# Optimization experiments

Hardware: AMD Instinct MI355X
Metric: run time of the kernel (lower is better)

The kernel has to match this reference:

```python
import jax, jax.numpy as jnp
import numpy as np

B, H, I = 64, 4096, 14336   # batch, hidden, expert intermediate
NLUT = 4096                 # 2**L_bits, L=12
W_SCALE = 0.02              # payload['W_scale'] (same for all three here)


def _rademacher(key, shape):
    return jnp.where(jax.random.bernoulli(key, 0.5, shape), 1.0, -1.0).astype(jnp.float32)


def setup_inputs() -> dict:
    key = jax.random.key(0)
    ks = jax.random.split(key, 14)
    inp = {
        "x": jax.random.normal(ks[0], (B, H), jnp.float32),
        "lut_gate": jax.random.normal(ks[1], (NLUT,), jnp.float32) * 0.05,
        "lut_up": jax.random.normal(ks[2], (NLUT,), jnp.float32) * 0.05,
        "lut_down": jax.random.normal(ks[3], (NLUT,), jnp.float32) * 0.05,
        "gate_walks": jax.random.randint(ks[4], (I, H), 0, NLUT, jnp.int32),
        "up_walks": jax.random.randint(ks[5], (I, H), 0, NLUT, jnp.int32),
        "down_walks": jax.random.randint(ks[6], (H, I), 0, NLUT, jnp.int32),
        "gate_sign_l": _rademacher(ks[7], (I,)),
        "gate_sign_r": _rademacher(ks[8], (H,)),
        "up_sign_l": _rademacher(ks[9], (I,)),
        "up_sign_r": _rademacher(ks[10], (H,)),
        "down_sign_l": _rademacher(ks[11], (H,)),
        "down_sign_r": _rademacher(ks[12], (I,)),
    }
    return inp


def _dequant(lut, walks, sign_l, sign_r):
    # trellis-walk LUT gather per weight element, then row/col signs and scalar scale
    # walks: (out, in) int codes; lut: (NLUT,)
    return (lut[walks] * sign_l[:, None] * sign_r[None, :]) * W_SCALE


def reference(x, lut_gate, lut_up, lut_down,
              gate_walks, up_walks, down_walks,
              gate_sign_l, gate_sign_r, up_sign_l, up_sign_r,
              down_sign_l, down_sign_r):
    W_gate = _dequant(lut_gate, gate_walks, gate_sign_l, gate_sign_r)  # (I, H)
    W_up = _dequant(lut_up, up_walks, up_sign_l, up_sign_r)            # (I, H)
    W_down = _dequant(lut_down, down_walks, down_sign_l, down_sign_r)  # (H, I)
    gate_out = jax.nn.silu(x @ W_gate.T)   # (B, I)
    up_out = x @ W_up.T                    # (B, I)
    hidden = gate_out * up_out
    return hidden @ W_down.T               # (B, H)
```

## Files before the change

### kernel.cpp

```cpp
#include <hip/hip_runtime.h>
#include <hip/hip_bf16.h>

#define HD   4096
#define ID   14336
#define NB   64
#define NLUTN 4096
#define KSPLIT 4

typedef __attribute__((ext_vector_type(8))) short short8;
typedef __attribute__((ext_vector_type(4))) float f32x4;

__device__ __forceinline__ unsigned short f2bf(float f) {
  __hip_bfloat16 h = __float2bfloat16(f);
  return __builtin_bit_cast(unsigned short, h);
}

__global__ __launch_bounds__(256) void prep_kernel(
    const float* __restrict__ x, const float* __restrict__ gsr,
    const float* __restrict__ usr,
    unsigned short* __restrict__ xg, unsigned short* __restrict__ xu)
{
  int t = blockIdx.x * 256 + threadIdx.x;
  float4 xv = ((const float4*)x)[t];
  int hs = t & (HD/4 - 1);
  float4 g = ((const float4*)gsr)[hs];
  float4 u = ((const float4*)usr)[hs];
  ushort4 og = make_ushort4(f2bf(xv.x*g.x), f2bf(xv.y*g.y), f2bf(xv.z*g.z), f2bf(xv.w*g.w));
  ushort4 ou = make_ushort4(f2bf(xv.x*u.x), f2bf(xv.y*u.y), f2bf(xv.z*u.z), f2bf(xv.w*u.w));
  ((ushort4*)xg)[t] = og;
  ((ushort4*)xu)[t] = ou;
}

__global__ __launch_bounds__(64) void gate_up_kernel(
    const int* __restrict__ gw, const int* __restrict__ uw,
    const float* __restrict__ lutg_f, const float* __restrict__ lutu_f,
    const unsigned short* __restrict__ xg, const unsigned short* __restrict__ xu,
    const float* __restrict__ gsl, const float* __restrict__ usl,
    const float* __restrict__ dsr,
    unsigned short* __restrict__ hidden)
{
  __shared__ unsigned short lutg[NLUTN];
  __shared__ unsigned short lutu[NLUTN];
  const int tid = threadIdx.x;

  #pragma unroll
  for (int i = tid; i < NLUTN/4; i += 64) {
    float4 g = ((const float4*)lutg_f)[i];
    float4 u = ((const float4*)lutu_f)[i];
    ((ushort4*)lutg)[i] = make_ushort4(f2bf(g.x), f2bf(g.y), f2bf(g.z), f2bf(g.w));
    ((ushort4*)lutu)[i] = make_ushort4(f2bf(u.x), f2bf(u.y), f2bf(u.z), f2bf(u.w));
  }
  __syncthreads();

  const int col  = tid & 15;
  const int quad = tid >> 4;
  const int m0   = blockIdx.x * 16;

  const int* gp = gw + (size_t)(m0 + col) * HD + quad * 8;
  const int* up = uw + (size_t)(m0 + col) * HD + quad * 8;
  const unsigned short* xgp[4];
  const unsigned short* xup[4];
  #pragma unroll
  for (int t = 0; t < 4; ++t) {
    xgp[t] = xg + (size_t)(t*16 + col) * HD + quad * 8;
    xup[t] = xu + (size_t)(t*16 + col) * HD + quad * 8;
  }

  const f32x4 z = {0.f, 0.f, 0.f, 0.f};
  f32x4 accg[4] = {z, z, z, z};
  f32x4 accu[4] = {z, z, z, z};

  for (int k0 = 0; k0 < HD; k0 += 32) {
    int4 ga = *(const int4*)(gp + k0);
    int4 gb = *(const int4*)(gp + k0 + 4);
    int4 ua = *(const int4*)(up + k0);
    int4 ub = *(const int4*)(up + k0 + 4);

    short8 afg, afu;
    afg[0] = (short)lutg[ga.x]; afg[1] = (short)lutg[ga.y];
    afg[2] = (short)lutg[ga.z]; afg[3] = (short)lutg[ga.w];
    afg[4] = (short)lutg[gb.x]; afg[5] = (short)lutg[gb.y];
    afg[6] = (short)lutg[gb.z]; afg[7] = (short)lutg[gb.w];
    afu[0] = (short)lutu[ua.x]; afu[1] = (short)lutu[ua.y];
    afu[2] = (short)lutu[ua.z]; afu[3] = (short)lutu[ua.w];
    afu[4] = (short)lutu[ub.x]; afu[5] = (short)lutu[ub.y];
    afu[6] = (short)lutu[ub.z]; afu[7] = (short)lutu[ub.w];

    #pragma unroll
    for (int t = 0; t < 4; ++t) {
      short8 bg = __builtin_bit_cast(short8, *(const int4*)(xgp[t] + k0));
      short8 bu = __builtin_bit_cast(short8, *(const int4*)(xup[t] + k0));
      accg[t] = __builtin_amdgcn_mfma_f32_16x16x32_bf16(afg, bg, accg[t], 0, 0, 0);
      accu[t] = __builtin_amdgcn_mfma_f32_16x16x32_bf16(afu, bu, accu[t], 0, 0, 0);
    }
  }

  const int mrow = m0 + quad * 4;
  float sg[4], su[4], sd[4];
  #pragma unroll
  for (int r = 0; r < 4; ++r) {
    sg[r] = 0.02f * gsl[mrow + r];
    su[r] = 0.02f * usl[mrow + r];
    sd[r] = dsr[mrow + r];
  }
  #pragma unroll
  for (int t = 0; t < 4; ++t) {
    int b = t*16 + col;
    ushort4 hv;
    float g0 = accg[t][0] * sg[0], u0 = accu[t][0] * su[0];
    float g1 = accg[t][1] * sg[1], u1 = accu[t][1] * su[1];
    float g2 = accg[t][2] * sg[2], u2 = accu[t][2] * su[2];
    float g3 = accg[t][3] * sg[3], u3 = accu[t][3] * su[3];
    hv.x = f2bf((g0 / (1.f + __expf(-g0))) * u0 * sd[0]);
    hv.y = f2bf((g1 / (1.f + __expf(-g1))) * u1 * sd[1]);
    hv.z = f2bf((g2 / (1.f + __expf(-g2))) * u2 * sd[2]);
    hv.w = f2bf((g3 / (1.f + __expf(-g3))) * u3 * sd[3]);
    *((ushort4*)(hidden + (size_t)b * ID + mrow)) = hv;
  }
}

__global__ __launch_bounds__(64) void down_kernel(
    const int* __restrict__ dw, const float* __restrict__ lutd_f,
    const unsigned short* __restrict__ hidden,
    const float* __restrict__ dsl,
    float* __restrict__ out)
{
  __shared__ unsigned short lutd[NLUTN];
  const int tid = threadIdx.x;
  #pragma unroll
  for (int i = tid; i < NLUTN/4; i += 64) {
    float4 d = ((const float4*)lutd_f)[i];
    ((ushort4*)lutd)[i] = make_ushort4(f2bf(d.x), f2bf(d.y), f2bf(d.z), f2bf(d.w));
  }
  __syncthreads();

  const int col  = tid & 15;
  const int quad = tid >> 4;
  const int m0   = blockIdx.x * 16;
  const int kbeg = blockIdx.y * (ID / KSPLIT);
  const int kend = kbeg + (ID / KSPLIT);

  const int* dp = dw + (size_t)(m0 + col) * ID + quad * 8;
  const unsigned short* hp[4];
  #pragma unroll
  for (int t = 0; t < 4; ++t)
    hp[t] = hidden + (size_t)(t*16 + col) * ID + quad * 8;

  const f32x4 z = {0.f, 0.f, 0.f, 0.f};
  f32x4 acc[4] = {z, z, z, z};

  for (int k0 = kbeg; k0 < kend; k0 += 32) {
    int4 da = *(const int4*)(dp + k0);
    int4 db = *(const int4*)(dp + k0 + 4);
    short8 af;
    af[0] = (short)lutd[da.x]; af[1] = (short)lutd[da.y];
    af[2] = (short)lutd[da.z]; af[3] = (short)lutd[da.w];
    af[4] = (short)lutd[db.x]; af[5] = (short)lutd[db.y];
    af[6] = (short)lutd[db.z]; af[7] = (short)lutd[db.w];
    #pragma unroll
    for (int t = 0; t < 4; ++t) {
      short8 bh = __builtin_bit_cast(short8, *(const int4*)(hp[t] + k0));
      acc[t] = __builtin_amdgcn_mfma_f32_16x16x32_bf16(af, bh, acc[t], 0, 0, 0);
    }
  }

  const int mrow = m0 + quad * 4;
  float sc[4];
  #pragma unroll
  for (int r = 0; r < 4; ++r) sc[r] = 0.02f * dsl[mrow + r];
  #pragma unroll
  for (int t = 0; t < 4; ++t) {
    int b = t*16 + col;
    #pragma unroll
    for (int r = 0; r < 4; ++r)
      atomicAdd(&out[(size_t)b * HD + mrow + r], acc[t][r] * sc[r]);
  }
}

extern "C" void kernel_launch(void* const* d_in, const int* in_sizes, int n_in,
                              void* d_out, int out_size, void* d_ws, size_t ws_size,
                              hipStream_t stream) {
  const float* x    = (const float*)d_in[0];
  const float* lutg = (const float*)d_in[1];
  const float* lutu = (const float*)d_in[2];
  const float* lutd = (const float*)d_in[3];
  const int*   gw   = (const int*)d_in[4];
  const int*   uw   = (const int*)d_in[5];
  const int*   dw   = (const int*)d_in[6];
  const float* gsl  = (const float*)d_in[7];
  const float* gsr  = (const float*)d_in[8];
  const float* usl  = (const float*)d_in[9];
  const float* usr  = (const float*)d_in[10];
  const float* dsl  = (const float*)d_in[11];
  const float* dsr  = (const float*)d_in[12];
  float* out = (float*)d_out;

  unsigned short* xg     = (unsigned short*)d_ws;
  unsigned short* xu     = xg + (size_t)NB * HD;
  unsigned short* hidden = xu + (size_t)NB * HD;

  hipMemsetAsync(d_out, 0, (size_t)NB * HD * sizeof(float), stream);
  prep_kernel<<<(NB*HD/4 + 255)/256, 256, 0, stream>>>(x, gsr, usr, xg, xu);
  gate_up_kernel<<<ID/16, 64, 0, stream>>>(gw, uw, lutg, lutu, xg, xu,
                                           gsl, usl, dsr, hidden);
  down_kernel<<<dim3(HD/16, KSPLIT), 64, 0, stream>>>(dw, lutd, hidden, dsl, out);
}
```

Measured before the change: 742.0 us.

## Split K across four waves per block with LDS reduction and prefetch walk codes

Both GEMM kernels now launch 256-thread blocks where each of four waves handles a quarter of the K range, and partial accumulators are summed through shared memory before the epilogue. This amortizes the per-block LUT conversion into LDS over four times more work and raises the number of waves per CU to hide the latency of the gathers and global loads. The loops also software-prefetch the next iteration's walk-code int4 loads. The cost is extra LDS for the reduction buffers, a block-wide barrier, and an idle epilogue for three of the four waves.

```diff
diff --git a/kernel.cpp b/kernel.cpp
--- a/kernel.cpp
+++ b/kernel.cpp
@@ -31,7 +31,7 @@
   ((ushort4*)xu)[t] = ou;
 }
 
-__global__ __launch_bounds__(64) void gate_up_kernel(
+__global__ __launch_bounds__(256, 4) void gate_up_kernel(
     const int* __restrict__ gw, const int* __restrict__ uw,
     const float* __restrict__ lutg_f, const float* __restrict__ lutu_f,
     const unsigned short* __restrict__ xg, const unsigned short* __restrict__ xu,
@@ -41,10 +41,14 @@
 {
   __shared__ unsigned short lutg[NLUTN];
   __shared__ unsigned short lutu[NLUTN];
-  const int tid = threadIdx.x;
-
-  #pragma unroll
-  for (int i = tid; i < NLUTN/4; i += 64) {
+  __shared__ f32x4 red[3][8][64];
+
+  const int tid  = threadIdx.x;
+  const int lane = tid & 63;
+  const int w    = tid >> 6;
+
+  #pragma unroll
+  for (int i = tid; i < NLUTN/4; i += 256) {
     float4 g = ((const float4*)lutg_f)[i];
     float4 u = ((const float4*)lutu_f)[i];
     ((ushort4*)lutg)[i] = make_ushort4(f2bf(g.x), f2bf(g.y), f2bf(g.z), f2bf(g.w));
@@ -52,9 +56,12 @@
   }
   __syncthreads();
 
-  const int col  = tid & 15;
-  const int quad = tid >> 4;
+  const int col  = lane & 15;
+  const int quad = lane >> 4;
   const int m0   = blockIdx.x * 16;
+
+  const int kbeg = w * (HD / 4);
+  const int kend = kbeg + (HD / 4);
 
   const int* gp = gw + (size_t)(m0 + col) * HD + quad * 8;
   const int* up = uw + (size_t)(m0 + col) * HD + quad * 8;
@@ -70,21 +77,28 @@
   f32x4 accg[4] = {z, z, z, z};
   f32x4 accu[4] = {z, z, z, z};
 
-  for (int k0 = 0; k0 < HD; k0 += 32) {
-    int4 ga = *(const int4*)(gp + k0);
-    int4 gb = *(const int4*)(gp + k0 + 4);
-    int4 ua = *(const int4*)(up + k0);
-    int4 ub = *(const int4*)(up + k0 + 4);
+  int4 cga = *(const int4*)(gp + kbeg);
+  int4 cgb = *(const int4*)(gp + kbeg + 4);
+  int4 cua = *(const int4*)(up + kbeg);
+  int4 cub = *(const int4*)(up + kbeg + 4);
+
+  for (int k0 = kbeg; k0 < kend; k0 += 32) {
+    int kn = k0 + 32;
+    if (kn >= kend) kn = kbeg;
+    int4 nga = *(const int4*)(gp + kn);
+    int4 ngb = *(const int4*)(gp + kn + 4);
+    int4 nua = *(const int4*)(up + kn);
+    int4 nub = *(const int4*)(up + kn + 4);
 
     short8 afg, afu;
-    afg[0] = (short)lutg[ga.x]; afg[1] = (short)lutg[ga.y];
-    afg[2] = (short)lutg[ga.z]; afg[3] = (short)lutg[ga.w];
-    afg[4] = (short)lutg[gb.x]; afg[5] = (short)lutg[gb.y];
-    afg[6] = (short)lutg[gb.z]; afg[7] = (short)lutg[gb.w];
-    afu[0] = (short)lutu[ua.x]; afu[1] = (short)lutu[ua.y];
-    afu[2] = (short)lutu[ua.z]; afu[3] = (short)lutu[ua.w];
-    afu[4] = (short)lutu[ub.x]; afu[5] = (short)lutu[ub.y];
-    afu[6] = (short)lutu[ub.z]; afu[7] = (short)lutu[ub.w];
+    afg[0] = (short)lutg[cga.x]; afg[1] = (short)lutg[cga.y];
+    afg[2] = (short)lutg[cga.z]; afg[3] = (short)lutg[cga.w];
+    afg[4] = (short)lutg[cgb.x]; afg[5] = (short)lutg[cgb.y];
+    afg[6] = (short)lutg[cgb.z]; afg[7] = (short)lutg[cgb.w];
+    afu[0] = (short)lutu[cua.x]; afu[1] = (short)lutu[cua.y];
+    afu[2] = (short)lutu[cua.z]; afu[3] = (short)lutu[cua.w];
+    afu[4] = (short)lutu[cub.x]; afu[5] = (short)lutu[cub.y];
+    afu[6] = (short)lutu[cub.z]; afu[7] = (short)lutu[cub.w];
 
     #pragma unroll
     for (int t = 0; t < 4; ++t) {
@@ -93,52 +107,79 @@
       accg[t] = __builtin_amdgcn_mfma_f32_16x16x32_bf16(afg, bg, accg[t], 0, 0, 0);
       accu[t] = __builtin_amdgcn_mfma_f32_16x16x32_bf16(afu, bu, accu[t], 0, 0, 0);
     }
-  }
-
-  const int mrow = m0 + quad * 4;
-  float sg[4], su[4], sd[4];
-  #pragma unroll
-  for (int r = 0; r < 4; ++r) {
-    sg[r] = 0.02f * gsl[mrow + r];
-    su[r] = 0.02f * usl[mrow + r];
-    sd[r] = dsr[mrow + r];
-  }
-  #pragma unroll
-  for (int t = 0; t < 4; ++t) {
-    int b = t*16 + col;
-    ushort4 hv;
-    float g0 = accg[t][0] * sg[0], u0 = accu[t][0] * su[0];
-    float g1 = accg[t][1] * sg[1], u1 = accu[t][1] * su[1];
-    float g2 = accg[t][2] * sg[2], u2 = accu[t][2] * su[2];
-    float g3 = accg[t][3] * sg[3], u3 = accu[t][3] * su[3];
-    hv.x = f2bf((g0 / (1.f + __expf(-g0))) * u0 * sd[0]);
-    hv.y = f2bf((g1 / (1.f + __expf(-g1))) * u1 * sd[1]);
-    hv.z = f2bf((g2 / (1.f + __expf(-g2))) * u2 * sd[2]);
-    hv.w = f2bf((g3 / (1.f + __expf(-g3))) * u3 * sd[3]);
-    *((ushort4*)(hidden + (size_t)b * ID + mrow)) = hv;
-  }
-}
-
-__global__ __launch_bounds__(64) void down_kernel(
+
+    cga = nga; cgb = ngb; cua = nua; cub = nub;
+  }
+
+  if (w > 0) {
+    #pragma unroll
+    for (int t = 0; t < 4; ++t) {
+      red[w-1][t][lane]     = accg[t];
+      red[w-1][4 + t][lane] = accu[t];
+    }
+  }
+  __syncthreads();
+  if (w == 0) {
+    #pragma unroll
+    for (int ww = 0; ww < 3; ++ww) {
+      #pragma unroll
+      for (int t = 0; t < 4; ++t) {
+        accg[t] += red[ww][t][lane];
+        accu[t] += red[ww][4 + t][lane];
+      }
+    }
+
+    const int mrow = m0 + quad * 4;
+    float sg[4], su[4], sd[4];
+    #pragma unroll
+    for (int r = 0; r < 4; ++r) {
+      sg[r] = 0.02f * gsl[mrow + r];
+      su[r] = 0.02f * usl[mrow + r];
+      sd[r] = dsr[mrow + r];
+    }
+    #pragma unroll
+    for (int t = 0; t < 4; ++t) {
+      int b = t*16 + col;
+      ushort4 hv;
+      float g0 = accg[t][0] * sg[0], u0 = accu[t][0] * su[0];
+      float g1 = accg[t][1] * sg[1], u1 = accu[t][1] * su[1];
+      float g2 = accg[t][2] * sg[2], u2 = accu[t][2] * su[2];
+      float g3 = accg[t][3] * sg[3], u3 = accu[t][3] * su[3];
+      hv.x = f2bf((g0 / (1.f + __expf(-g0))) * u0 * sd[0]);
+      hv.y = f2bf((g1 / (1.f + __expf(-g1))) * u1 * sd[1]);
+      hv.z = f2bf((g2 / (1.f + __expf(-g2))) * u2 * sd[2]);
+      hv.w = f2bf((g3 / (1.f + __expf(-g3))) * u3 * sd[3]);
+      *((ushort4*)(hidden + (size_t)b * ID + mrow)) = hv;
+    }
+  }
+}
+
+__global__ __launch_bounds__(256, 4) void down_kernel(
     const int* __restrict__ dw, const float* __restrict__ lutd_f,
     const unsigned short* __restrict__ hidden,
     const float* __restrict__ dsl,
     float* __restrict__ out)
 {
   __shared__ unsigned short lutd[NLUTN];
-  const int tid = threadIdx.x;
-  #pragma unroll
-  for (int i = tid; i < NLUTN/4; i += 64) {
+  __shared__ f32x4 red[3][4][64];
+
+  const int tid  = threadIdx.x;
+  const int lane = tid & 63;
+  const int w    = tid >> 6;
+
+  #pragma unroll
+  for (int i = tid; i < NLUTN/4; i += 256) {
     float4 d = ((const float4*)lutd_f)[i];
     ((ushort4*)lutd)[i] = make_ushort4(f2bf(d.x), f2bf(d.y), f2bf(d.z), f2bf(d.w));
   }
   __syncthreads();
 
-  const int col  = tid & 15;
-  const int quad = tid >> 4;
+  const int col  = lane & 15;
+  const int quad = lane >> 4;
   const int m0   = blockIdx.x * 16;
-  const int kbeg = blockIdx.y * (ID / KSPLIT);
-  const int kend = kbeg + (ID / KSPLIT);
+  const int kchunk = ID / KSPLIT;
+  const int kbeg = blockIdx.y * kchunk + w * (kchunk / 4);
+  const int kend = kbeg + kchunk / 4;
 
   const int* dp = dw + (size_t)(m0 + col) * ID + quad * 8;
   const unsigned short* hp[4];
@@ -149,31 +190,53 @@
   const f32x4 z = {0.f, 0.f, 0.f, 0.f};
   f32x4 acc[4] = {z, z, z, z};
 
+  int4 cda = *(const int4*)(dp + kbeg);
+  int4 cdb = *(const int4*)(dp + kbeg + 4);
+
   for (int k0 = kbeg; k0 < kend; k0 += 32) {
-    int4 da = *(const int4*)(dp + k0);
-    int4 db = *(const int4*)(dp + k0 + 4);
+    int kn = k0 + 32;
+    if (kn >= kend) kn = kbeg;
+    int4 nda = *(const int4*)(dp + kn);
+    int4 ndb = *(const int4*)(dp + kn + 4);
+
     short8 af;
-    af[0] = (short)lutd[da.x]; af[1] = (short)lutd[da.y];
-    af[2] = (short)lutd[da.z]; af[3] = (short)lutd[da.w];
-    af[4] = (short)lutd[db.x]; af[5] = (short)lutd[db.y];
-    af[6] = (short)lutd[db.z]; af[7] = (short)lutd[db.w];
+    af[0] = (short)lutd[cda.x]; af[1] = (short)lutd[cda.y];
+    af[2] = (short)lutd[cda.z]; af[3] = (short)lutd[cda.w];
+    af[4] = (short)lutd[cdb.x]; af[5] = (short)lutd[cdb.y];
+    af[6] = (short)lutd[cdb.z]; af[7] = (short)lutd[cdb.w];
+
     #pragma unroll
     for (int t = 0; t < 4; ++t) {
       short8 bh = __builtin_bit_cast(short8, *(const int4*)(hp[t] + k0));
       acc[t] = __builtin_amdgcn_mfma_f32_16x16x32_bf16(af, bh, acc[t], 0, 0, 0);
     }
-  }
-
-  const int mrow = m0 + quad * 4;
-  float sc[4];
-  #pragma unroll
-  for (int r = 0; r < 4; ++r) sc[r] = 0.02f * dsl[mrow + r];
-  #pragma unroll
-  for (int t = 0; t < 4; ++t) {
-    int b = t*16 + col;
-    #pragma unroll
-    for (int r = 0; r < 4; ++r)
-      atomicAdd(&out[(size_t)b * HD + mrow + r], acc[t][r] * sc[r]);
+
+    cda = nda; cdb = ndb;
+  }
+
+  if (w > 0) {
+    #pragma unroll
+    for (int t = 0; t < 4; ++t) red[w-1][t][lane] = acc[t];
+  }
+  __syncthreads();
+  if (w == 0) {
+    #pragma unroll
+    for (int ww = 0; ww < 3; ++ww) {
+      #pragma unroll
+      for (int t = 0; t < 4; ++t) acc[t] += red[ww][t][lane];
+    }
+
+    const int mrow = m0 + quad * 4;
+    float sc[4];
+    #pragma unroll
+    for (int r = 0; r < 4; ++r) sc[r] = 0.02f * dsl[mrow + r];
+    #pragma unroll
+    for (int t = 0; t < 4; ++t) {
+      int b = t*16 + col;
+      #pragma unroll
+      for (int r = 0; r < 4; ++r)
+        atomicAdd(&out[(size_t)b * HD + mrow + r], acc[t][r] * sc[r]);
+    }
   }
 }
 
@@ -201,7 +264,7 @@
 
   hipMemsetAsync(d_out, 0, (size_t)NB * HD * sizeof(float), stream);
   prep_kernel<<<(NB*HD/4 + 255)/256, 256, 0, stream>>>(x, gsr, usr, xg, xu);
-  gate_up_kernel<<<ID/16, 64, 0, stream>>>(gw, uw, lutg, lutu, xg, xu,
-                                           gsl, usl, dsr, hidden);
-  down_kernel<<<dim3(HD/16, KSPLIT), 64, 0, stream>>>(dw, lutd, hidden, dsl, out);
-}
+  gate_up_kernel<<<ID/16, 256, 0, stream>>>(gw, uw, lutg, lutu, xg, xu,
+                                            gsl, usl, dsr, hidden);
+  down_kernel<<<dim3(HD/16, KSPLIT), 256, 0, stream>>>(dw, lutd, hidden, dsl, out);
+}
```

Measured after the change: 758.7 us. 1.02x slower.
